# Kernel tuning notes

Measured on AMD Instinct MI355X. Metric: run time of the kernel, lower is better.

## Reference

```python
import jax, jax.numpy as jnp
import numpy as np

B, S, H, D = 4, 2048, 16, 64
E = H * D  # embed_dim = 1024


def setup_inputs() -> dict:
    key = jax.random.key(0)
    kq, kk, kv, kw, kb = jax.random.split(key, 5)
    query = jax.random.normal(kq, (B, S, H, D), dtype=jnp.float32)
    key_t = jax.random.normal(kk, (B, S, H, D), dtype=jnp.float32)
    value = jax.random.normal(kv, (B, S, H, D), dtype=jnp.float32)
    qkv_proj = jnp.zeros((1,), dtype=jnp.float32)  # unused arg in original forward
    # causal mask (0 = masked), matching masked_fill(attn_mask == 0, -inf)
    attn_mask = jnp.tril(jnp.ones((S, S), dtype=jnp.int32))
    bound = 1.0 / np.sqrt(E)
    out_w = jax.random.uniform(kw, (E, E), jnp.float32, -bound, bound)
    out_b = jax.random.uniform(kb, (E,), jnp.float32, -bound, bound)
    return {"query": query, "key": key_t, "value": value, "qkv_proj": qkv_proj,
            "attn_mask": attn_mask, "out_w": out_w, "out_b": out_b}


def reference(query, key, value, qkv_proj, attn_mask, out_w, out_b):
    # flatten heads: module does single-head attention over embed_dim
    q = query.reshape(B, S, E) * (float(E) ** -0.5)  # scaling uses embed_dim, per source
    k = key.reshape(B, S, E)
    v = value.reshape(B, S, E)
    scores = jnp.einsum('bqe,bke->bqk', q, k)  # [B,S,S]
    scores = jnp.where(attn_mask[None, :, :] == 0, -jnp.inf, scores)
    # safe softmax: subtract max, exp, normalize
    probs = jax.nn.softmax(scores, axis=-1)
    attn_out = jnp.einsum('bqk,bke->bqe', probs, v)  # [B,S,E]
    return attn_out @ out_w.T + out_b
```

## Files before the change

kernel.cpp:

```cpp
#include <hip/hip_runtime.h>


typedef __attribute__((ext_vector_type(8))) short bf16x8;
typedef __attribute__((ext_vector_type(4))) float floatx4;

#define MFMA16(a, b, c) __builtin_amdgcn_mfma_f32_16x16x32_bf16((a), (b), (c), 0, 0, 0)

#define B_ 4
#define S_ 2048
#define E_ 1024

static __device__ __forceinline__ unsigned short f2bf(float f) {
  unsigned int u = __float_as_uint(f);
  u += 0x7FFFu + ((u >> 16) & 1u);
  return (unsigned short)(u >> 16);
}
static __device__ __forceinline__ float bf2f(unsigned short h) {
  return __uint_as_float(((unsigned int)h) << 16);
}

#define STAGE_TILE_64(dst, srcbase, LD, k0, w, l)                              \
  _Pragma("unroll")                                                            \
  for (int i_ = 0; i_ < 4; ++i_) {                                             \
    int c_ = i_ * 256 + (w) * 64 + (l);                                        \
    int row_ = c_ >> 3, cg_ = c_ & 7;                                          \
    int col_ = (cg_ ^ (row_ & 7)) * 8;                                         \
    __builtin_amdgcn_global_load_lds(                                          \
        (const __attribute__((address_space(1))) unsigned int*)((srcbase) +    \
            (size_t)row_ * (LD) + (k0) + col_),                                \
        (__attribute__((address_space(3))) unsigned int*)((dst) +              \
            (size_t)(i_ * 256 + (w) * 64) * 8),                                \
        16, 0, 0);                                                             \
  }

static __device__ __forceinline__ const bf16x8* frag_at(
    const unsigned short* base, int row, int cg) {
  return (const bf16x8*)(base + (size_t)row * 64 + ((cg ^ (row & 7)) * 8));
}

__global__ void cvt_all_kernel(const float* __restrict__ Q,
                               const float* __restrict__ K,
                               const float* __restrict__ W,
                               unsigned short* __restrict__ Qbf,
                               unsigned short* __restrict__ Kbf,
                               unsigned short* __restrict__ Wbf) {
  const int nQK = (B_ * S_ * E_) / 4;
  const int nW  = (E_ * E_) / 4;
  const int total = 2 * nQK + nW;
  int i = blockIdx.x * blockDim.x + threadIdx.x;
  int stride = gridDim.x * blockDim.x;
  for (; i < total; i += stride) {
    const float* src; unsigned short* dst; float sc; int j;
    if (i < nQK)            { src = Q; dst = Qbf; sc = 0.03125f; j = i; }
    else if (i < 2 * nQK)   { src = K; dst = Kbf; sc = 1.0f; j = i - nQK; }
    else                    { src = W; dst = Wbf; sc = 1.0f; j = i - 2 * nQK; }
    float4 v = ((const float4*)src)[j];
    ushort4 o;
    o.x = f2bf(v.x * sc); o.y = f2bf(v.y * sc);
    o.z = f2bf(v.z * sc); o.w = f2bf(v.w * sc);
    ((ushort4*)dst)[j] = o;
  }
}

__global__ void transpose_v_kernel(const float* __restrict__ V,
                                   unsigned short* __restrict__ Vt) {
  __shared__ float tile[32][33];
  int bid = blockIdx.x;
  int eb = (bid & 31) * 32;
  int sb = ((bid >> 5) & 63) * 32;
  int b  = bid >> 11;
  int tx = threadIdx.x & 31, ty = threadIdx.x >> 5;
  const float* src = V + ((size_t)(b * S_ + sb)) * E_ + eb;
#pragma unroll
  for (int i = 0; i < 4; ++i) {
    int sl = ty + i * 8;
    tile[sl][tx] = src[(size_t)sl * E_ + tx];
  }
  __syncthreads();
  unsigned short* dst = Vt + ((size_t)(b * E_ + eb)) * S_ + sb;
#pragma unroll
  for (int i = 0; i < 4; ++i) {
    int el = ty + i * 8;
    dst[(size_t)el * S_ + tx] = f2bf(tile[tx][el]);
  }
}

__global__ __launch_bounds__(256, 3) void qk_kernel(
    const unsigned short* __restrict__ A,
    const unsigned short* __restrict__ Bw,
    unsigned short* __restrict__ SP) {
  __shared__ unsigned short At[128 * 64];
  __shared__ unsigned short Bt[128 * 64];
  const int bid0 = blockIdx.x;
  const int bid = (bid0 & 7) * 68 + (bid0 >> 3);
  const int b = bid / 136;
  const int ti = bid - b * 136;
  float fr = sqrtf(8.0f * (float)ti + 1.0f);
  int trow = (int)((fr - 1.0f) * 0.5f);
  if ((trow + 1) * (trow + 2) / 2 <= ti) ++trow;
  else if (trow * (trow + 1) / 2 > ti) --trow;
  const int tcol = ti - trow * (trow + 1) / 2;
  const int bm = trow * 128, bn = tcol * 128;

  const int tid = threadIdx.x;
  const int w = tid >> 6, l = tid & 63;
  const int l15 = l & 15, l4 = l >> 4;
  const int wr = w >> 1, wc = w & 1;
  const unsigned short* Ab = A + (size_t)b * S_ * E_ + (size_t)bm * E_;
  const unsigned short* Bb = Bw + (size_t)b * S_ * E_ + (size_t)bn * E_;

  floatx4 acc[4][4];
#pragma unroll
  for (int m = 0; m < 4; ++m)
#pragma unroll
    for (int n = 0; n < 4; ++n) acc[m][n] = (floatx4)0.0f;

  for (int k0 = 0; k0 < E_; k0 += 64) {
    STAGE_TILE_64(At, Ab, E_, k0, w, l)
    STAGE_TILE_64(Bt, Bb, E_, k0, w, l)
    __syncthreads();
#pragma unroll
    for (int h = 0; h < 2; ++h) {
      bf16x8 af[4], bfv[4];
#pragma unroll
      for (int mf = 0; mf < 4; ++mf)
        af[mf] = *frag_at(At, wr * 64 + mf * 16 + l15, h * 4 + l4);
#pragma unroll
      for (int nf = 0; nf < 4; ++nf)
        bfv[nf] = *frag_at(Bt, wc * 64 + nf * 16 + l15, h * 4 + l4);
#pragma unroll
      for (int mf = 0; mf < 4; ++mf)
#pragma unroll
        for (int nf = 0; nf < 4; ++nf)
          acc[mf][nf] = MFMA16(af[mf], bfv[nf], acc[mf][nf]);
    }
    __syncthreads();
  }

  unsigned short* Cb = SP + (size_t)b * S_ * S_;
#pragma unroll
  for (int mf = 0; mf < 4; ++mf)
#pragma unroll
    for (int nf = 0; nf < 4; ++nf)
#pragma unroll
      for (int r = 0; r < 4; ++r) {
        int row = bm + wr * 64 + mf * 16 + l4 * 4 + r;
        int col = bn + wc * 64 + nf * 16 + l15;
        float p = (col <= row) ? __expf(acc[mf][nf][r]) : 0.0f;
        Cb[(size_t)row * S_ + col] = f2bf(p);
      }
}

__global__ __launch_bounds__(256) void rowsum_kernel(
    const unsigned short* __restrict__ P, float* __restrict__ rsum) {
  const int gw = blockIdx.x * 4 + (threadIdx.x >> 6);
  const int b = gw >> 11, q = gw & 2047;
  const int l = threadIdx.x & 63;
  const unsigned short* row = P + ((size_t)(b * S_ + q)) * S_;
  const int bound = ((q >> 7) + 1) * 128;
  float sum = 0.0f;
  for (int c0 = l * 8; c0 < bound; c0 += 512) {
    bf16x8 v = *(const bf16x8*)(row + c0);
#pragma unroll
    for (int e = 0; e < 8; ++e) sum += bf2f((unsigned short)v[e]);
  }
  sum += __shfl_xor(sum, 1);
  sum += __shfl_xor(sum, 2);
  sum += __shfl_xor(sum, 4);
  sum += __shfl_xor(sum, 8);
  sum += __shfl_xor(sum, 16);
  sum += __shfl_xor(sum, 32);
  if (l == 0) rsum[gw] = sum;
}

__global__ __launch_bounds__(256, 2) void pv_kernel(
    const unsigned short* __restrict__ P,
    const unsigned short* __restrict__ Vt,
    const float* __restrict__ rsumG,
    unsigned short* __restrict__ Abf) {
  __shared__ unsigned short At[2][128 * 64];
  __shared__ unsigned short Bt[2][128 * 64];
  const int bid = blockIdx.x;
  const int b = bid >> 7;
  int mt = (bid >> 3) & 15;
  const int nt = bid & 7;
  if (bid >= 256) mt = 15 - mt;
  const int bm = mt * 128, bn = nt * 128;

  const int tid = threadIdx.x;
  const int w = tid >> 6, l = tid & 63;
  const int l15 = l & 15, l4 = l >> 4;
  const int wr = w >> 1, wc = w & 1;
  const unsigned short* Ab = P + (size_t)b * S_ * S_ + (size_t)bm * S_;
  const unsigned short* Bb = Vt + (size_t)b * E_ * S_ + (size_t)bn * S_;

  floatx4 acc[4][4];
#pragma unroll
  for (int m = 0; m < 4; ++m)
#pragma unroll
    for (int n = 0; n < 4; ++n) acc[m][n] = (floatx4)0.0f;

  const int NT = (mt + 1) * 2;
  STAGE_TILE_64(At[0], Ab, S_, 0, w, l)
  STAGE_TILE_64(Bt[0], Bb, S_, 0, w, l)
  __syncthreads();
  int cur = 0;
  for (int t = 0; t < NT; ++t) {
    if (t + 1 < NT) {
      STAGE_TILE_64(At[cur ^ 1], Ab, S_, (t + 1) * 64, w, l)
      STAGE_TILE_64(Bt[cur ^ 1], Bb, S_, (t + 1) * 64, w, l)
    }
#pragma unroll
    for (int h = 0; h < 2; ++h) {
      bf16x8 af[4], bfv[4];
#pragma unroll
      for (int mf = 0; mf < 4; ++mf)
        af[mf] = *frag_at(At[cur], wr * 64 + mf * 16 + l15, h * 4 + l4);
#pragma unroll
      for (int nf = 0; nf < 4; ++nf)
        bfv[nf] = *frag_at(Bt[cur], wc * 64 + nf * 16 + l15, h * 4 + l4);
#pragma unroll
      for (int mf = 0; mf < 4; ++mf)
#pragma unroll
        for (int nf = 0; nf < 4; ++nf)
          acc[mf][nf] = MFMA16(af[mf], bfv[nf], acc[mf][nf]);
    }
    __syncthreads();
    cur ^= 1;
  }

  unsigned short* Cb = Abf + (size_t)b * S_ * E_;
  const float* rs = rsumG + (size_t)b * S_ + bm;
#pragma unroll
  for (int mf = 0; mf < 4; ++mf) {
    float inv[4];
#pragma unroll
    for (int r = 0; r < 4; ++r)
      inv[r] = 1.0f / rs[wr * 64 + mf * 16 + l4 * 4 + r];
#pragma unroll
    for (int nf = 0; nf < 4; ++nf)
#pragma unroll
      for (int r = 0; r < 4; ++r) {
        int row = bm + wr * 64 + mf * 16 + l4 * 4 + r;
        int col = bn + wc * 64 + nf * 16 + l15;
        Cb[(size_t)row * E_ + col] = f2bf(acc[mf][nf][r] * inv[r]);
      }
  }
}

__global__ __launch_bounds__(256, 2) void proj_kernel(
    const unsigned short* __restrict__ A,
    const unsigned short* __restrict__ Bw,
    const float* __restrict__ bias,
    float* __restrict__ C) {
  __shared__ unsigned short At[2][128 * 64];
  __shared__ unsigned short Bt[2][128 * 64];
  const int bid0 = blockIdx.x;
  const int bid = (bid0 & 7) * 64 + (bid0 >> 3);
  const int tid = threadIdx.x;
  const int w = tid >> 6, l = tid & 63;
  const int l15 = l & 15, l4 = l >> 4;
  const int wr = w >> 1, wc = w & 1;
  const int bm = (bid >> 3) * 128;
  const int bn = (bid & 7) * 128;
  const unsigned short* Ab = A + (size_t)bm * E_;
  const unsigned short* Bb = Bw + (size_t)bn * E_;

  floatx4 acc[4][4];
#pragma unroll
  for (int m = 0; m < 4; ++m)
#pragma unroll
    for (int n = 0; n < 4; ++n) acc[m][n] = (floatx4)0.0f;

  const int NT = E_ / 64;
  STAGE_TILE_64(At[0], Ab, E_, 0, w, l)
  STAGE_TILE_64(Bt[0], Bb, E_, 0, w, l)
  __syncthreads();
  int cur = 0;
  for (int t = 0; t < NT; ++t) {
    if (t + 1 < NT) {
      STAGE_TILE_64(At[cur ^ 1], Ab, E_, (t + 1) * 64, w, l)
      STAGE_TILE_64(Bt[cur ^ 1], Bb, E_, (t + 1) * 64, w, l)
    }
#pragma unroll
    for (int h = 0; h < 2; ++h) {
      bf16x8 af[4], bfv[4];
#pragma unroll
      for (int mf = 0; mf < 4; ++mf)
        af[mf] = *frag_at(At[cur], wr * 64 + mf * 16 + l15, h * 4 + l4);
#pragma unroll
      for (int nf = 0; nf < 4; ++nf)
        bfv[nf] = *frag_at(Bt[cur], wc * 64 + nf * 16 + l15, h * 4 + l4);
#pragma unroll
      for (int mf = 0; mf < 4; ++mf)
#pragma unroll
        for (int nf = 0; nf < 4; ++nf)
          acc[mf][nf] = MFMA16(af[mf], bfv[nf], acc[mf][nf]);
    }
    __syncthreads();
    cur ^= 1;
  }

  float bv[4];
#pragma unroll
  for (int nf = 0; nf < 4; ++nf) bv[nf] = bias[bn + wc * 64 + nf * 16 + l15];
#pragma unroll
  for (int mf = 0; mf < 4; ++mf)
#pragma unroll
    for (int nf = 0; nf < 4; ++nf)
#pragma unroll
      for (int r = 0; r < 4; ++r) {
        int row = bm + wr * 64 + mf * 16 + l4 * 4 + r;
        int col = bn + wc * 64 + nf * 16 + l15;
        C[(size_t)row * E_ + col] = acc[mf][nf][r] + bv[nf];
      }
}

extern "C" void kernel_launch(void* const* d_in, const int* in_sizes, int n_in,
                              void* d_out, int out_size, void* d_ws, size_t ws_size,
                              hipStream_t stream) {
  const float* Q    = (const float*)d_in[0];
  const float* Kf   = (const float*)d_in[1];
  const float* V    = (const float*)d_in[2];
  const float* W    = (const float*)d_in[5];
  const float* bias = (const float*)d_in[6];
  float* out = (float*)d_out;
  (void)ws_size;

  char* ws = (char*)d_ws;
  unsigned short* Qbf = (unsigned short*)(ws);
  unsigned short* Kbf = (unsigned short*)(ws + (size_t)(16u << 20));
  unsigned short* Vt  = (unsigned short*)(ws + (size_t)(32u << 20));
  unsigned short* Wbf = (unsigned short*)(ws + (size_t)(48u << 20));
  unsigned short* SP  = (unsigned short*)(ws + (size_t)(50u << 20));
  float*          rsum = (float*)(ws + (size_t)(82u << 20));
  unsigned short* Abf = Kbf;

  cvt_all_kernel<<<4096, 256, 0, stream>>>(Q, Kf, W, Qbf, Kbf, Wbf);
  transpose_v_kernel<<<B_ * (S_ / 32) * (E_ / 32), 256, 0, stream>>>(V, Vt);

  qk_kernel<<<B_ * 136, 256, 0, stream>>>(Qbf, Kbf, SP);
  rowsum_kernel<<<B_ * S_ / 4, 256, 0, stream>>>(SP, rsum);
  pv_kernel<<<B_ * 16 * 8, 256, 0, stream>>>(SP, Vt, rsum, Abf);
  proj_kernel<<<(B_ * S_ / 128) * (E_ / 128), 256, 0, stream>>>(Abf, Wbf, bias, out);
}
```

Before: 119.4 us.

## Fuse row-sum into QK epilogue and remap PV block schedule

The softmax row-sum reduction moves into the QK kernel's epilogue. Each tile reduces its exp values with shuffles and shared memory and writes per-tile partial sums, so the separate rowsum kernel no longer has to re-read the whole P matrix. The PV kernel now adds those partials (up to 16 per row) before normalizing. Its block-to-tile mapping is also reordered to interleave batches and pair heavy and light row tiles, which should improve load balance and locality. In exchange the partials are computed from fp32 values, not the rounded bf16 ones, and the PV epilogue does extra scalar loads.

```diff
diff --git a/kernel.cpp b/kernel.cpp
--- a/kernel.cpp
+++ b/kernel.cpp
@@ -88,9 +88,11 @@
 __global__ __launch_bounds__(256, 3) void qk_kernel(
     const unsigned short* __restrict__ A,
     const unsigned short* __restrict__ Bw,
-    unsigned short* __restrict__ SP) {
+    unsigned short* __restrict__ SP,
+    float* __restrict__ rsp) {
   __shared__ unsigned short At[128 * 64];
   __shared__ unsigned short Bt[128 * 64];
+  __shared__ float rs_l[2][128];
   const int bid0 = blockIdx.x;
   const int bid = (bid0 & 7) * 68 + (bid0 >> 3);
   const int b = bid / 136;
@@ -137,6 +139,9 @@
     __syncthreads();
   }
 
+  float ps[16];
+#pragma unroll
+  for (int i = 0; i < 16; ++i) ps[i] = 0.0f;
   unsigned short* Cb = SP + (size_t)b * S_ * S_;
 #pragma unroll
   for (int mf = 0; mf < 4; ++mf)
@@ -147,44 +152,44 @@
         int row = bm + wr * 64 + mf * 16 + l4 * 4 + r;
         int col = bn + wc * 64 + nf * 16 + l15;
         float p = (col <= row) ? __expf(acc[mf][nf][r]) : 0.0f;
+        ps[mf * 4 + r] += p;
         Cb[(size_t)row * S_ + col] = f2bf(p);
       }
-}
-
-__global__ __launch_bounds__(256) void rowsum_kernel(
-    const unsigned short* __restrict__ P, float* __restrict__ rsum) {
-  const int gw = blockIdx.x * 4 + (threadIdx.x >> 6);
-  const int b = gw >> 11, q = gw & 2047;
-  const int l = threadIdx.x & 63;
-  const unsigned short* row = P + ((size_t)(b * S_ + q)) * S_;
-  const int bound = ((q >> 7) + 1) * 128;
-  float sum = 0.0f;
-  for (int c0 = l * 8; c0 < bound; c0 += 512) {
-    bf16x8 v = *(const bf16x8*)(row + c0);
-#pragma unroll
-    for (int e = 0; e < 8; ++e) sum += bf2f((unsigned short)v[e]);
-  }
-  sum += __shfl_xor(sum, 1);
-  sum += __shfl_xor(sum, 2);
-  sum += __shfl_xor(sum, 4);
-  sum += __shfl_xor(sum, 8);
-  sum += __shfl_xor(sum, 16);
-  sum += __shfl_xor(sum, 32);
-  if (l == 0) rsum[gw] = sum;
+#pragma unroll
+  for (int i = 0; i < 16; ++i) {
+    float s = ps[i];
+    s += __shfl_xor(s, 1);
+    s += __shfl_xor(s, 2);
+    s += __shfl_xor(s, 4);
+    s += __shfl_xor(s, 8);
+    ps[i] = s;
+  }
+  if (l15 == 0) {
+#pragma unroll
+    for (int mf = 0; mf < 4; ++mf)
+#pragma unroll
+      for (int r = 0; r < 4; ++r)
+        rs_l[wc][wr * 64 + mf * 16 + l4 * 4 + r] = ps[mf * 4 + r];
+  }
+  __syncthreads();
+  if (tid < 128)
+    rsp[((size_t)(b * S_ + bm + tid)) * 17 + tcol] = rs_l[0][tid] + rs_l[1][tid];
 }
 
 __global__ __launch_bounds__(256, 2) void pv_kernel(
     const unsigned short* __restrict__ P,
     const unsigned short* __restrict__ Vt,
-    const float* __restrict__ rsumG,
+    const float* __restrict__ rsp,
     unsigned short* __restrict__ Abf) {
   __shared__ unsigned short At[2][128 * 64];
   __shared__ unsigned short Bt[2][128 * 64];
-  const int bid = blockIdx.x;
-  const int b = bid >> 7;
-  int mt = (bid >> 3) & 15;
-  const int nt = bid & 7;
-  if (bid >= 256) mt = 15 - mt;
+  const int bid0 = blockIdx.x;
+  const int x = bid0 & 7;
+  const int j = bid0 >> 3;
+  const int b = x >> 1;
+  const int nt = (x & 1) * 4 + (j & 3);
+  const int r2 = j >> 2;
+  const int mt = (r2 < 8) ? r2 : 23 - r2;
   const int bm = mt * 128, bn = nt * 128;
 
   const int tid = threadIdx.x;
@@ -230,13 +235,17 @@
   }
 
   unsigned short* Cb = Abf + (size_t)b * S_ * E_;
-  const float* rs = rsumG + (size_t)b * S_ + bm;
+  const float* rp = rsp + ((size_t)(b * S_ + bm)) * 17;
 #pragma unroll
   for (int mf = 0; mf < 4; ++mf) {
     float inv[4];
 #pragma unroll
-    for (int r = 0; r < 4; ++r)
-      inv[r] = 1.0f / rs[wr * 64 + mf * 16 + l4 * 4 + r];
+    for (int r = 0; r < 4; ++r) {
+      int rl = wr * 64 + mf * 16 + l4 * 4 + r;
+      float s = 0.0f;
+      for (int t = 0; t <= mt; ++t) s += rp[rl * 17 + t];
+      inv[r] = 1.0f / s;
+    }
 #pragma unroll
     for (int nf = 0; nf < 4; ++nf)
 #pragma unroll
@@ -333,14 +342,13 @@
   unsigned short* Vt  = (unsigned short*)(ws + (size_t)(32u << 20));
   unsigned short* Wbf = (unsigned short*)(ws + (size_t)(48u << 20));
   unsigned short* SP  = (unsigned short*)(ws + (size_t)(50u << 20));
-  float*          rsum = (float*)(ws + (size_t)(82u << 20));
+  float*          rsp = (float*)(ws + (size_t)(82u << 20));
   unsigned short* Abf = Kbf;
 
   cvt_all_kernel<<<4096, 256, 0, stream>>>(Q, Kf, W, Qbf, Kbf, Wbf);
   transpose_v_kernel<<<B_ * (S_ / 32) * (E_ / 32), 256, 0, stream>>>(V, Vt);
 
-  qk_kernel<<<B_ * 136, 256, 0, stream>>>(Qbf, Kbf, SP);
-  rowsum_kernel<<<B_ * S_ / 4, 256, 0, stream>>>(SP, rsum);
-  pv_kernel<<<B_ * 16 * 8, 256, 0, stream>>>(SP, Vt, rsum, Abf);
+  qk_kernel<<<B_ * 136, 256, 0, stream>>>(Qbf, Kbf, SP, rsp);
+  pv_kernel<<<B_ * 16 * 8, 256, 0, stream>>>(SP, Vt, rsp, Abf);
   proj_kernel<<<(B_ * S_ / 128) * (E_ / 128), 256, 0, stream>>>(Abf, Wbf, bias, out);
 }
```

After: 133.7 us. 1.12x slower.
